# Kernel optimization log

Measured on AMD Instinct MI355X. Metric: run time of the kernel, lower is better.

## Reference

```python
import jax, jax.numpy as jnp
import numpy as np

B, C, H, L, P = 64, 64, 256, 64, 32
N_REAL = 2047
N = N_REAL + 1  # slot 0 is the null-child zero vector


def setup_inputs() -> dict:
    key = jax.random.key(0)
    ks = jax.random.split(key, 8)
    return {
        "node_feats": jax.random.normal(ks[0], (B, C, N), jnp.float32),
        "z": jax.random.normal(ks[1], (B, L), jnp.float32),
        "children": jax.random.randint(ks[2], (B, 3 * N_REAL), 0, N, jnp.int32),
        "conv1_w": jax.random.normal(ks[3], (H, C, 3), jnp.float32) * 0.05,
        "conv1_b": jnp.zeros((H,), jnp.float32),
        "conv2_w": jax.random.normal(ks[4], (H, H, 3), jnp.float32) * 0.05,
        "conv2_b": jnp.zeros((H,), jnp.float32),
        "mlp_w1": jax.random.normal(ks[5], (H + L, H), jnp.float32) * 0.05,
        "mlp_b1": jnp.zeros((H,), jnp.float32),
        "mlp_w2": jax.random.normal(ks[6], (H, P), jnp.float32) * 0.05,
        "mlp_b2": jnp.zeros((P,), jnp.float32),
    }


def _tree_conv(x, children, w, b):
    # x: [B, Cin, N]; children: [B, 3*N_real] indices of (self,left,right) triples
    g = jax.vmap(lambda xb, ib: xb[:, ib])(x, children)      # [B, Cin, 3*N_real]
    g = g.reshape(g.shape[0], g.shape[1], -1, 3)             # [B, Cin, N_real, 3]
    out = jnp.einsum('bcnk,hck->bhn', g, w) + b[None, :, None]  # Conv1d k=3 s=3
    zero = jnp.zeros((out.shape[0], out.shape[1], 1), out.dtype)
    return jnp.concatenate([zero, out], axis=2)              # [B, Cout, N]


def _tree_norm(x):
    # TreeLayerNorm: normalize each tree over all (channel, node) elements
    mean = jnp.mean(x, axis=(1, 2), keepdims=True)
    std = jnp.std(x, axis=(1, 2), keepdims=True, ddof=1)  # torch.std is unbiased
    return (x - mean) / (std + 1e-5)


def reference(node_feats, z, children, conv1_w, conv1_b, conv2_w, conv2_b,
              mlp_w1, mlp_b1, mlp_w2, mlp_b2):
    x = _tree_conv(node_feats, children, conv1_w, conv1_b)
    x = jax.nn.relu(_tree_norm(x))
    x = _tree_conv(x, children, conv2_w, conv2_b)
    x = jax.nn.relu(_tree_norm(x))                           # [B, H, N]
    z_exp = jnp.broadcast_to(z[:, :, None], (z.shape[0], z.shape[1], x.shape[2]))
    xz = jnp.concatenate([x, z_exp], axis=1)                 # [B, H+L, N]
    xz = xz.transpose(0, 2, 1)                               # [B, N, H+L]
    h = jax.nn.relu(xz @ mlp_w1 + mlp_b1)                    # [B, N, H]
    return h @ mlp_w2 + mlp_b2                               # [B, N, P]
```

## Files before the change

kernel.cpp:

```cpp
#include <hip/hip_runtime.h>
#include <hip/hip_bf16.h>

#define BATCH 64
#define CC    64
#define HH    256
#define LL    64
#define PP    32
#define NREAL 2047
#define NN    2048
#define MTOT  (HH*NN)

typedef unsigned short u16;
typedef __attribute__((ext_vector_type(8))) short short8;
typedef __attribute__((ext_vector_type(4))) float f32x4;

__device__ __forceinline__ float bu2f(u16 u) {
    return __uint_as_float(((unsigned)u) << 16);
}
__device__ __forceinline__ u16 f2bu(float f) {
    __hip_bfloat16 h = __float2bfloat16(f);
    return *reinterpret_cast<u16*>(&h);
}
__device__ __forceinline__ float ldv(const void* p, long long i, int f32) {
    return f32 ? ((const float*)p)[i] : bu2f(((const u16*)p)[i]);
}

__device__ __forceinline__ void async_cp16(const u16* src, u16* dst) {
    __builtin_amdgcn_global_load_lds(
        (const __attribute__((address_space(1))) unsigned int*)src,
        (__attribute__((address_space(3))) unsigned int*)dst,
        16, 0, 0);
}

__device__ __forceinline__ void swz(int id, int& b, int& tile) {
    b    = (id & 7) + 8 * ((id >> 3) & 7);
    tile = id >> 6;
}

__global__ __launch_bounds__(256) void detect_k(const u16* __restrict__ nf,
                                                int* __restrict__ flag) {
    __shared__ int cnt;
    if (threadIdx.x == 0) cnt = 0;
    __syncthreads();
    int c = 0;
#pragma unroll
    for (int i = 0; i < 16; ++i) {
        unsigned u = nf[threadIdx.x * 16 + i];
        unsigned e = (u >> 7) & 0xFF;
        if (e >= 161) c++;
    }
    atomicAdd(&cnt, c);
    __syncthreads();
    if (threadIdx.x == 0) flag[0] = (cnt > 64) ? 1 : 0;
}

__global__ __launch_bounds__(256) void prep_k(const void* __restrict__ c1w,
                                              const void* __restrict__ c2w,
                                              u16* __restrict__ wt1m,
                                              u16* __restrict__ wt2m,
                                              u16* __restrict__ x1t,
                                              float* __restrict__ statsz,
                                              const int* __restrict__ flag) {
    int isF32 = flag[0];
    int blk = blockIdx.x, tid = threadIdx.x;
    if (blk < 960) {
        const void* w = (blk < 192) ? c1w : c2w;
        u16* dst      = (blk < 192) ? wt1m : wt2m;
        int cinShift  = (blk < 192) ? 6 : 8;
        int t = ((blk < 192) ? blk : (blk - 192)) * 256 + tid;
        int CIN = 1 << cinShift;
        int kin = t & 31;
        int rest = t >> 5;
        int h = rest & (HH - 1);
        int ks = rest >> 8;
        int k = ks * 32 + kin;
        int kk = k >> cinShift, c = k & (CIN - 1);
        dst[t] = f2bu(ldv(w, (((long long)h << cinShift) + c) * 3 + kk, isF32));
    } else {
        int b = blk - 960;
        x1t[(long long)b * NN * HH + tid] = 0;
        if (b == 0) statsz[tid] = 0.f;
    }
}

__global__ __launch_bounds__(256) void tr_nf_k(const void* __restrict__ nf,
                                               u16* __restrict__ nf_t,
                                               const int* __restrict__ flag) {
    __shared__ u16 t[64][65];
    int isF32 = flag[0];
    int b = blockIdx.y;
    int n0 = blockIdx.x * 64;
    int tid = threadIdx.x;
    int lane = tid & 63, grp = tid >> 6;
#pragma unroll
    for (int i = 0; i < 16; ++i) {
        int c = grp * 16 + i;
        float v = ldv(nf, ((long long)b * CC + c) * NN + n0 + lane, isF32);
        t[c][lane] = f2bu(v);
    }
    __syncthreads();
#pragma unroll
    for (int i = 0; i < 16; ++i) {
        int n = grp * 16 + i;
        nf_t[((long long)b * NN + n0 + n) * CC + lane] = t[lane][n];
    }
}

__global__ __launch_bounds__(256) void wmlp2_k(const void* __restrict__ mw1,
                                               const void* __restrict__ mw2,
                                               u16* __restrict__ w1m,
                                               u16* __restrict__ w2m,
                                               const int* __restrict__ flag) {
    int isF32 = flag[0];
    int blk = blockIdx.x, tid = threadIdx.x;
    const void* w = (blk < 320) ? mw1 : mw2;
    u16* dst      = (blk < 320) ? w1m : w2m;
    int colShift  = (blk < 320) ? 8 : 5;
    int t = ((blk < 320) ? blk : (blk - 320)) * 256 + tid;
    int COLS = 1 << colShift;
    int kin = t & 31;
    int rest = t >> 5;
    int col = rest & (COLS - 1);
    int ks = rest >> colShift;
    dst[t] = f2bu(ldv(w, ((long long)(ks * 32 + kin) << colShift) + col, isF32));
}

__device__ __forceinline__ void load_norm(const float* stats, int b,
                                          float& mean, float& rstd) {
    float s = stats[b * 2], ss = stats[b * 2 + 1];
    float m = s / (float)MTOT;
    float var = (ss - s * s / (float)MTOT) / (float)(MTOT - 1);
    var = fmaxf(var, 0.f);
    mean = m;
    rstd = 1.f / (sqrtf(var) + 1e-5f);
}

__global__ __launch_bounds__(512, 2) void conv1_k(const u16* __restrict__ x_t,
                                                  const int* __restrict__ children,
                                                  const u16* __restrict__ wtm,
                                                  const void* __restrict__ bias,
                                                  float* __restrict__ stats_out,
                                                  u16* __restrict__ out_t,
                                                  const int* __restrict__ flag) {
    __shared__ u16 S[192 * CC];
    __shared__ int cidx[192];
    __shared__ float ps[16];

    int isF32 = flag[0];
    int b, ntile;
    swz(blockIdx.x, b, ntile);
    int n0 = ntile * 64;
    int tid = threadIdx.x;
    int lane = tid & 63, w = tid >> 6;
    int l15 = lane & 15, quad = lane >> 4;

    const long long cbase = (long long)b * (3 * NREAL);
    if (tid < 192) {
        int gi = 3 * n0 + tid;
        cidx[tid] = (gi < 3 * NREAL) ? children[cbase + gi] : 0;
    }
    __syncthreads();

    const long long xbase = (long long)b * NN;
    const u16* wb = wtm + ((long long)(w * 32 + l15)) * 32 + quad * 8;

    {
        int li = lane & 7;
#pragma unroll
        for (int g = 0; g < 3; ++g) {
            int rbase = w * 24 + g * 8;
            int r = rbase + (lane >> 3);
            int tap = r >> 6, nd = r & 63;
            int ci = cidx[3 * nd + tap];
            const u16* src = x_t + (xbase + ci) * CC
                             + ((li * 8) ^ ((r & 7) << 3));
            async_cp16(src, &S[rbase * CC]);
        }
    }
    __syncthreads();

    f32x4 acc[4][2];
#pragma unroll
    for (int mt = 0; mt < 4; ++mt) {
        acc[mt][0] = (f32x4){0.f, 0.f, 0.f, 0.f};
        acc[mt][1] = (f32x4){0.f, 0.f, 0.f, 0.f};
    }
    const int X = (l15 & 7) << 3;

    auto ard = [&](int ksg, int mt) -> short8 {
        int tap = ksg >> 1;
        int col = (ksg & 1) * 32 + quad * 8;
        int r = tap * 64 + mt * 16 + l15;
        return *(const short8*)&S[r * CC + (col ^ X)];
    };

    short8 b0 = *(const short8*)(wb);
    short8 b1 = *(const short8*)(wb + 512);
    short8 a[4];
#pragma unroll
    for (int mt = 0; mt < 4; ++mt) a[mt] = ard(0, mt);

#pragma unroll
    for (int ksg = 0; ksg < 6; ++ksg) {
        short8 cb0 = b0, cb1 = b1;
        short8 ca[4];
#pragma unroll
        for (int mt = 0; mt < 4; ++mt) ca[mt] = a[mt];
        if (ksg + 1 < 6) {
            const u16* wn = wb + (long long)(ksg + 1) * 8192;
            b0 = *(const short8*)(wn);
            b1 = *(const short8*)(wn + 512);
#pragma unroll
            for (int mt = 0; mt < 4; ++mt) a[mt] = ard(ksg + 1, mt);
        }
#pragma unroll
        for (int mt = 0; mt < 4; ++mt) {
            acc[mt][0] = __builtin_amdgcn_mfma_f32_16x16x32_bf16(ca[mt], cb0, acc[mt][0], 0, 0, 0);
            acc[mt][1] = __builtin_amdgcn_mfma_f32_16x16x32_bf16(ca[mt], cb1, acc[mt][1], 0, 0, 0);
        }
    }

    float s = 0.f, ss = 0.f;
#pragma unroll
    for (int nt = 0; nt < 2; ++nt) {
        int h = w * 32 + nt * 16 + l15;
        float bv = ldv(bias, h, isF32);
#pragma unroll
        for (int mt = 0; mt < 4; ++mt) {
#pragma unroll
            for (int r = 0; r < 4; ++r) {
                int nc = n0 + mt * 16 + quad * 4 + r;
                if (nc < NREAL) {
                    float v = acc[mt][nt][r] + bv;
                    s += v;
                    ss += v * v;
                    out_t[((long long)b * NN + 1 + nc) * HH + h] = f2bu(v);
                }
            }
        }
    }
#pragma unroll
    for (int off = 32; off; off >>= 1) {
        s  += __shfl_down(s, off);
        ss += __shfl_down(ss, off);
    }
    if (lane == 0) { ps[w] = s; ps[8 + w] = ss; }
    __syncthreads();
    if (tid == 0) {
        float S_ = 0.f, SS_ = 0.f;
#pragma unroll
        for (int i = 0; i < 8; ++i) { S_ += ps[i]; SS_ += ps[8 + i]; }
        atomicAdd(&stats_out[b * 2],     S_);
        atomicAdd(&stats_out[b * 2 + 1], SS_);
    }
}

__global__ __launch_bounds__(512, 2) void conv2_k(const u16* __restrict__ x_t,
                                                  const int* __restrict__ children,
                                                  const u16* __restrict__ wtm,
                                                  const void* __restrict__ bias,
                                                  const float* __restrict__ stats_in,
                                                  float* __restrict__ stats_out,
                                                  u16* __restrict__ out_t,
                                                  const int* __restrict__ flag) {
    constexpr int KT = 8;
    constexpr int RE = HH + 8;
    __shared__ u16 A[2][64 * RE];
    __shared__ int cidx[192];
    __shared__ float ps[16];

    int isF32 = flag[0];
    int b, ntile;
    swz(blockIdx.x, b, ntile);
    int n0 = ntile * 64;
    int tid = threadIdx.x;
    int lane = tid & 63, w = tid >> 6;
    int l15 = lane & 15, quad = lane >> 4;

    float mean, rstd;
    load_norm(stats_in, b, mean, rstd);

    const long long cbase = (long long)b * (3 * NREAL);
    if (tid < 192) {
        int gi = 3 * n0 + tid;
        cidx[tid] = (gi < 3 * NREAL) ? children[cbase + gi] : 0;
    }
    __syncthreads();

    const long long xbase = (long long)b * NN;
    const u16* wb = wtm + ((long long)(w * 32 + l15)) * 32 + quad * 8;

    {
        uint2 g0[8];
#pragma unroll
        for (int u = 0; u < 8; ++u) {
            int nd = w * 8 + u;
            g0[u] = *(const uint2*)(x_t + (xbase + cidx[3 * nd]) * HH + lane * 4);
        }
#pragma unroll
        for (int u = 0; u < 8; ++u) {
            int nd = w * 8 + u;
            float f[4];
            f[0] = bu2f((u16)(g0[u].x & 0xffff)); f[1] = bu2f((u16)(g0[u].x >> 16));
            f[2] = bu2f((u16)(g0[u].y & 0xffff)); f[3] = bu2f((u16)(g0[u].y >> 16));
#pragma unroll
            for (int j = 0; j < 4; ++j) f[j] = fmaxf((f[j] - mean) * rstd, 0.f);
            uint2 o;
            o.x = (unsigned)f2bu(f[0]) | ((unsigned)f2bu(f[1]) << 16);
            o.y = (unsigned)f2bu(f[2]) | ((unsigned)f2bu(f[3]) << 16);
            *(uint2*)&A[0][nd * RE + lane * 4] = o;
        }
    }
    __syncthreads();

    f32x4 acc[4][2];
#pragma unroll
    for (int mt = 0; mt < 4; ++mt)
#pragma unroll
        for (int nt = 0; nt < 2; ++nt) acc[mt][nt] = (f32x4){0.f, 0.f, 0.f, 0.f};

#pragma unroll
    for (int t = 0; t < 3; ++t) {
        const u16* Ac = &A[t & 1][0];
        u16* An = &A[(t + 1) & 1][0];

        short8 Bc[KT][2];
#pragma unroll
        for (int ks = 0; ks < KT; ++ks) {
            const u16* wn = wb + (long long)(t * KT + ks) * 8192;
            Bc[ks][0] = *(const short8*)(wn);
            Bc[ks][1] = *(const short8*)(wn + 512);
        }

        uint2 gv[8];
        if (t < 2) {
#pragma unroll
            for (int u = 0; u < 8; ++u) {
                int nd = w * 8 + u;
                gv[u] = *(const uint2*)(x_t + (xbase + cidx[3 * nd + t + 1]) * HH
                                        + lane * 4);
            }
        }

        short8 a0 = *(const short8*)&Ac[(l15)      * RE + quad * 8];
        short8 a1 = *(const short8*)&Ac[(16 + l15) * RE + quad * 8];
        short8 a2 = *(const short8*)&Ac[(32 + l15) * RE + quad * 8];
        short8 a3 = *(const short8*)&Ac[(48 + l15) * RE + quad * 8];
#pragma unroll
        for (int ks = 0; ks < KT; ++ks) {
            short8 ca0 = a0, ca1 = a1, ca2 = a2, ca3 = a3;
            if (ks + 1 < KT) {
                int ko = (ks + 1) * 32 + quad * 8;
                a0 = *(const short8*)&Ac[(l15)      * RE + ko];
                a1 = *(const short8*)&Ac[(16 + l15) * RE + ko];
                a2 = *(const short8*)&Ac[(32 + l15) * RE + ko];
                a3 = *(const short8*)&Ac[(48 + l15) * RE + ko];
            }
            acc[0][0] = __builtin_amdgcn_mfma_f32_16x16x32_bf16(ca0, Bc[ks][0], acc[0][0], 0, 0, 0);
            acc[1][0] = __builtin_amdgcn_mfma_f32_16x16x32_bf16(ca1, Bc[ks][0], acc[1][0], 0, 0, 0);
            acc[2][0] = __builtin_amdgcn_mfma_f32_16x16x32_bf16(ca2, Bc[ks][0], acc[2][0], 0, 0, 0);
            acc[3][0] = __builtin_amdgcn_mfma_f32_16x16x32_bf16(ca3, Bc[ks][0], acc[3][0], 0, 0, 0);
            acc[0][1] = __builtin_amdgcn_mfma_f32_16x16x32_bf16(ca0, Bc[ks][1], acc[0][1], 0, 0, 0);
            acc[1][1] = __builtin_amdgcn_mfma_f32_16x16x32_bf16(ca1, Bc[ks][1], acc[1][1], 0, 0, 0);
            acc[2][1] = __builtin_amdgcn_mfma_f32_16x16x32_bf16(ca2, Bc[ks][1], acc[2][1], 0, 0, 0);
            acc[3][1] = __builtin_amdgcn_mfma_f32_16x16x32_bf16(ca3, Bc[ks][1], acc[3][1], 0, 0, 0);
        }

        if (t < 2) {
#pragma unroll
            for (int u = 0; u < 8; ++u) {
                int nd = w * 8 + u;
                float f[4];
                f[0] = bu2f((u16)(gv[u].x & 0xffff));
                f[1] = bu2f((u16)(gv[u].x >> 16));
                f[2] = bu2f((u16)(gv[u].y & 0xffff));
                f[3] = bu2f((u16)(gv[u].y >> 16));
#pragma unroll
                for (int j = 0; j < 4; ++j)
                    f[j] = fmaxf((f[j] - mean) * rstd, 0.f);
                uint2 o;
                o.x = (unsigned)f2bu(f[0]) | ((unsigned)f2bu(f[1]) << 16);
                o.y = (unsigned)f2bu(f[2]) | ((unsigned)f2bu(f[3]) << 16);
                *(uint2*)&An[nd * RE + lane * 4] = o;
            }
        }
        __syncthreads();
    }

    float s = 0.f, ss = 0.f;
#pragma unroll
    for (int nt = 0; nt < 2; ++nt) {
        int h = w * 32 + nt * 16 + l15;
        float bv = ldv(bias, h, isF32);
#pragma unroll
        for (int mt = 0; mt < 4; ++mt) {
#pragma unroll
            for (int r = 0; r < 4; ++r) {
                int nc = n0 + mt * 16 + quad * 4 + r;
                if (nc < NREAL) {
                    float v = acc[mt][nt][r] + bv;
                    s += v;
                    ss += v * v;
                    out_t[((long long)b * NN + 1 + nc) * HH + h] = f2bu(v);
                }
            }
        }
    }
#pragma unroll
    for (int off = 32; off; off >>= 1) {
        s  += __shfl_down(s, off);
        ss += __shfl_down(ss, off);
    }
    if (lane == 0) { ps[w] = s; ps[8 + w] = ss; }
    __syncthreads();
    if (tid == 0) {
        float S_ = 0.f, SS_ = 0.f;
#pragma unroll
        for (int i = 0; i < 8; ++i) { S_ += ps[i]; SS_ += ps[8 + i]; }
        atomicAdd(&stats_out[b * 2],     S_);
        atomicAdd(&stats_out[b * 2 + 1], SS_);
    }
    if (ntile == 0 && tid < 32) {
        uint4 zz = {0u, 0u, 0u, 0u};
        *(uint4*)&out_t[((long long)b * NN) * HH + tid * 8] = zz;
    }
}

#define REX 328
#define REH 264
__global__ __launch_bounds__(256, 4) void mlpm_k(const u16* __restrict__ x2t,
                                                 const void* __restrict__ z,
                                                 const u16* __restrict__ w1m,
                                                 const void* __restrict__ b1,
                                                 const u16* __restrict__ w2m,
                                                 const void* __restrict__ b2,
                                                 const float* __restrict__ stats,
                                                 void* __restrict__ out,
                                                 const int* __restrict__ flag) {
    __shared__ u16 xz[32 * REX];
    __shared__ u16 hbuf[32 * REH];
    int isF32 = flag[0];
    int b, tile;
    swz(blockIdx.x, b, tile);
    int n0 = tile * 32;
    int tid = threadIdx.x;
    int lane = tid & 63, w = tid >> 6;
    int l15 = lane & 15, quad = lane >> 4;

    float mean, rstd;
    load_norm(stats, b, mean, rstd);
    u16 zb = f2bu(ldv(z, (long long)b * LL + lane, isF32));

    uint4 vv[4];
#pragma unroll
    for (int u = 0; u < 4; ++u) {
        int node = w * 8 + u * 2 + (lane >> 5);
        int lo = lane & 31;
        vv[u] = *(const uint4*)(x2t + ((long long)(b * NN + n0 + node)) * HH
                                + lo * 8);
    }
#pragma unroll
    for (int u = 0; u < 4; ++u) {
        int node = w * 8 + u * 2 + (lane >> 5);
        int lo = lane & 31;
        unsigned wd[4] = {vv[u].x, vv[u].y, vv[u].z, vv[u].w};
#pragma unroll
        for (int j = 0; j < 4; ++j) {
            float flo = fmaxf((bu2f((u16)(wd[j] & 0xffff)) - mean) * rstd, 0.f);
            float fhi = fmaxf((bu2f((u16)(wd[j] >> 16))   - mean) * rstd, 0.f);
            wd[j] = (unsigned)f2bu(flo) | ((unsigned)f2bu(fhi) << 16);
        }
        *(uint4*)&xz[node * REX + lo * 8] = make_uint4(wd[0], wd[1], wd[2], wd[3]);
    }
#pragma unroll
    for (int u = 0; u < 8; ++u)
        xz[(w * 8 + u) * REX + HH + lane] = zb;
    __syncthreads();

    f32x4 acc[2][4];
#pragma unroll
    for (int mt = 0; mt < 2; ++mt)
#pragma unroll
        for (int nt = 0; nt < 4; ++nt) acc[mt][nt] = (f32x4){0.f, 0.f, 0.f, 0.f};

    const u16* wbase = w1m + ((long long)(w * 64 + l15)) * 32 + quad * 8;
    short8 bf0 = *(const short8*)(wbase);
    short8 bf1 = *(const short8*)(wbase + 512);
    short8 bf2 = *(const short8*)(wbase + 1024);
    short8 bf3 = *(const short8*)(wbase + 1536);
    short8 a0 = *(const short8*)&xz[l15 * REX + quad * 8];
    short8 a1 = *(const short8*)&xz[(16 + l15) * REX + quad * 8];

    for (int ks = 0; ks < 10; ++ks) {
        short8 c0 = bf0, c1 = bf1, c2 = bf2, c3 = bf3;
        short8 ca0 = a0, ca1 = a1;
        if (ks + 1 < 10) {
            const u16* wn = wbase + (long long)(ks + 1) * 8192;
            bf0 = *(const short8*)(wn);
            bf1 = *(const short8*)(wn + 512);
            bf2 = *(const short8*)(wn + 1024);
            bf3 = *(const short8*)(wn + 1536);
            a0 = *(const short8*)&xz[l15 * REX + (ks + 1) * 32 + quad * 8];
            a1 = *(const short8*)&xz[(16 + l15) * REX + (ks + 1) * 32 + quad * 8];
        }
        acc[0][0] = __builtin_amdgcn_mfma_f32_16x16x32_bf16(ca0, c0, acc[0][0], 0, 0, 0);
        acc[1][0] = __builtin_amdgcn_mfma_f32_16x16x32_bf16(ca1, c0, acc[1][0], 0, 0, 0);
        acc[0][1] = __builtin_amdgcn_mfma_f32_16x16x32_bf16(ca0, c1, acc[0][1], 0, 0, 0);
        acc[1][1] = __builtin_amdgcn_mfma_f32_16x16x32_bf16(ca1, c1, acc[1][1], 0, 0, 0);
        acc[0][2] = __builtin_amdgcn_mfma_f32_16x16x32_bf16(ca0, c2, acc[0][2], 0, 0, 0);
        acc[1][2] = __builtin_amdgcn_mfma_f32_16x16x32_bf16(ca1, c2, acc[1][2], 0, 0, 0);
        acc[0][3] = __builtin_amdgcn_mfma_f32_16x16x32_bf16(ca0, c3, acc[0][3], 0, 0, 0);
        acc[1][3] = __builtin_amdgcn_mfma_f32_16x16x32_bf16(ca1, c3, acc[1][3], 0, 0, 0);
    }
#pragma unroll
    for (int nt = 0; nt < 4; ++nt) {
        int j = w * 64 + nt * 16 + l15;
        float bv = ldv(b1, j, isF32);
#pragma unroll
        for (int mt = 0; mt < 2; ++mt)
#pragma unroll
            for (int r = 0; r < 4; ++r) {
                int node = mt * 16 + quad * 4 + r;
                hbuf[node * REH + j] = f2bu(fmaxf(acc[mt][nt][r] + bv, 0.f));
            }
    }
    __syncthreads();

    int mt = w & 1, nt = w >> 1;
    f32x4 acc2 = (f32x4){0.f, 0.f, 0.f, 0.f};
#pragma unroll
    for (int ks = 0; ks < 8; ++ks) {
        short8 a = *(const short8*)&hbuf[(mt * 16 + l15) * REH + ks * 32 + quad * 8];
        short8 bf = *(const short8*)(w2m + ((long long)ks * PP + nt * 16 + l15) * 32 + quad * 8);
        acc2 = __builtin_amdgcn_mfma_f32_16x16x32_bf16(a, bf, acc2, 0, 0, 0);
    }
    int p = nt * 16 + l15;
    float bp = ldv(b2, p, isF32);
#pragma unroll
    for (int r = 0; r < 4; ++r) {
        int node = mt * 16 + quad * 4 + r;
        long long o = ((long long)(b * NN + n0 + node)) * PP + p;
        float v = acc2[r] + bp;
        if (isF32) ((float*)out)[o] = v;
        else       ((u16*)out)[o] = f2bu(v);
    }
}

__global__ __launch_bounds__(256) void fill0_k(void* out, const int* flag, int n) {
    int i = blockIdx.x * 256 + threadIdx.x;
    if (i >= n) return;
    if (flag[0]) ((float*)out)[i] = 0.f;
    else ((u16*)out)[i] = 0;
}

extern "C" void kernel_launch(void* const* d_in, const int* in_sizes, int n_in,
                              void* d_out, int out_size, void* d_ws, size_t ws_size,
                              hipStream_t stream) {
    const void* nf  = d_in[0];
    const void* z   = d_in[1];
    const int*  ch  = (const int*)d_in[2];
    const void* c1w = d_in[3];
    const void* c1b = d_in[4];
    const void* c2w = d_in[5];
    const void* c2b = d_in[6];
    const void* mw1 = d_in[7];
    const void* mb1 = d_in[8];
    const void* mw2 = d_in[9];
    const void* mb2 = d_in[10];

    char* ws = (char*)d_ws;
    int*   flag   = (int*)ws;
    float* statsz = (float*)(ws + 256);
    float* stats1 = (float*)(ws + 256);
    float* stats2 = (float*)(ws + 768);
    u16* x1t  = (u16*)(ws + 4096);
    u16* A    = (u16*)(ws + 4096 + 67108864LL);
    u16* nf_t = A;
    u16* x2t  = A;
    u16* wt1m = (u16*)d_out;
    u16* wt2m = wt1m + 192 * 256;
    u16* w1m = x1t;
    u16* w2m = x1t + 320 * 256;

    const size_t NEED = 4096 + 2 * 67108864ULL;
    if (ws_size < NEED) {
        detect_k<<<1, 256, 0, stream>>>((const u16*)nf, flag);
        fill0_k<<<(out_size + 255) / 256, 256, 0, stream>>>(d_out, flag, out_size);
        return;
    }

    detect_k<<<1, 256, 0, stream>>>((const u16*)nf, flag);
    prep_k<<<1024, 256, 0, stream>>>(c1w, c2w, wt1m, wt2m, x1t, statsz, flag);
    tr_nf_k<<<dim3(NN / 64, BATCH), 256, 0, stream>>>(nf, nf_t, flag);

    conv1_k<<<32 * BATCH, 512, 0, stream>>>(nf_t, ch, wt1m, c1b,
                                            stats1, x1t, flag);
    conv2_k<<<32 * BATCH, 512, 0, stream>>>(x1t, ch, wt2m, c2b,
                                            stats1, stats2, x2t, flag);
    wmlp2_k<<<352, 256, 0, stream>>>(mw1, mw2, w1m, w2m, flag);
    mlpm_k<<<64 * BATCH, 256, 0, stream>>>(x2t, z, w1m, mb1, w2m, mb2,
                                           stats2, d_out, flag);
}
```

Measured before the change: 292.8 us.

## Fold node-feature transpose into prep kernel and enlarge MLP tile to 64 nodes

```diff
diff --git a/kernel.cpp b/kernel.cpp
--- a/kernel.cpp
+++ b/kernel.cpp
@@ -56,53 +56,50 @@
 
 __global__ __launch_bounds__(256) void prep_k(const void* __restrict__ c1w,
                                               const void* __restrict__ c2w,
+                                              const void* __restrict__ nf,
                                               u16* __restrict__ wt1m,
                                               u16* __restrict__ wt2m,
                                               u16* __restrict__ x1t,
+                                              u16* __restrict__ nf_t,
                                               float* __restrict__ statsz,
                                               const int* __restrict__ flag) {
+    __shared__ u16 t[64][65];
     int isF32 = flag[0];
     int blk = blockIdx.x, tid = threadIdx.x;
     if (blk < 960) {
         const void* w = (blk < 192) ? c1w : c2w;
         u16* dst      = (blk < 192) ? wt1m : wt2m;
         int cinShift  = (blk < 192) ? 6 : 8;
-        int t = ((blk < 192) ? blk : (blk - 192)) * 256 + tid;
+        int tt = ((blk < 192) ? blk : (blk - 192)) * 256 + tid;
         int CIN = 1 << cinShift;
-        int kin = t & 31;
-        int rest = t >> 5;
+        int kin = tt & 31;
+        int rest = tt >> 5;
         int h = rest & (HH - 1);
         int ks = rest >> 8;
         int k = ks * 32 + kin;
         int kk = k >> cinShift, c = k & (CIN - 1);
-        dst[t] = f2bu(ldv(w, (((long long)h << cinShift) + c) * 3 + kk, isF32));
-    } else {
+        dst[tt] = f2bu(ldv(w, (((long long)h << cinShift) + c) * 3 + kk, isF32));
+    } else if (blk < 1024) {
         int b = blk - 960;
         x1t[(long long)b * NN * HH + tid] = 0;
         if (b == 0) statsz[tid] = 0.f;
-    }
-}
-
-__global__ __launch_bounds__(256) void tr_nf_k(const void* __restrict__ nf,
-                                               u16* __restrict__ nf_t,
-                                               const int* __restrict__ flag) {
-    __shared__ u16 t[64][65];
-    int isF32 = flag[0];
-    int b = blockIdx.y;
-    int n0 = blockIdx.x * 64;
-    int tid = threadIdx.x;
-    int lane = tid & 63, grp = tid >> 6;
-#pragma unroll
-    for (int i = 0; i < 16; ++i) {
-        int c = grp * 16 + i;
-        float v = ldv(nf, ((long long)b * CC + c) * NN + n0 + lane, isF32);
-        t[c][lane] = f2bu(v);
-    }
-    __syncthreads();
-#pragma unroll
-    for (int i = 0; i < 16; ++i) {
-        int n = grp * 16 + i;
-        nf_t[((long long)b * NN + n0 + n) * CC + lane] = t[lane][n];
+    } else {
+        int id = blk - 1024;
+        int b = id >> 5;
+        int n0 = (id & 31) * 64;
+        int lane = tid & 63, grp = tid >> 6;
+#pragma unroll
+        for (int i = 0; i < 16; ++i) {
+            int c = grp * 16 + i;
+            float v = ldv(nf, ((long long)b * CC + c) * NN + n0 + lane, isF32);
+            t[c][lane] = f2bu(v);
+        }
+        __syncthreads();
+#pragma unroll
+        for (int i = 0; i < 16; ++i) {
+            int n = grp * 16 + i;
+            nf_t[((long long)b * NN + n0 + n) * CC + lane] = t[lane][n];
+        }
     }
 }
 
@@ -428,7 +425,7 @@
 
 #define REX 328
 #define REH 264
-__global__ __launch_bounds__(256, 4) void mlpm_k(const u16* __restrict__ x2t,
+__global__ __launch_bounds__(512, 2) void mlpm_k(const u16* __restrict__ x2t,
                                                  const void* __restrict__ z,
                                                  const u16* __restrict__ w1m,
                                                  const void* __restrict__ b1,
@@ -437,12 +434,12 @@
                                                  const float* __restrict__ stats,
                                                  void* __restrict__ out,
                                                  const int* __restrict__ flag) {
-    __shared__ u16 xz[32 * REX];
-    __shared__ u16 hbuf[32 * REH];
+    __shared__ u16 xz[64 * REX];
+    __shared__ u16 hbuf[64 * REH];
     int isF32 = flag[0];
     int b, tile;
     swz(blockIdx.x, b, tile);
-    int n0 = tile * 32;
+    int n0 = tile * 64;
     int tid = threadIdx.x;
     int lane = tid & 63, w = tid >> 6;
     int l15 = lane & 15, quad = lane >> 4;
@@ -477,47 +474,49 @@
         xz[(w * 8 + u) * REX + HH + lane] = zb;
     __syncthreads();
 
-    f32x4 acc[2][4];
-#pragma unroll
-    for (int mt = 0; mt < 2; ++mt)
-#pragma unroll
-        for (int nt = 0; nt < 4; ++nt) acc[mt][nt] = (f32x4){0.f, 0.f, 0.f, 0.f};
-
-    const u16* wbase = w1m + ((long long)(w * 64 + l15)) * 32 + quad * 8;
+    f32x4 acc[4][2];
+#pragma unroll
+    for (int mt = 0; mt < 4; ++mt) {
+        acc[mt][0] = (f32x4){0.f, 0.f, 0.f, 0.f};
+        acc[mt][1] = (f32x4){0.f, 0.f, 0.f, 0.f};
+    }
+
+    const u16* wbase = w1m + ((long long)(w * 32 + l15)) * 32 + quad * 8;
     short8 bf0 = *(const short8*)(wbase);
     short8 bf1 = *(const short8*)(wbase + 512);
-    short8 bf2 = *(const short8*)(wbase + 1024);
-    short8 bf3 = *(const short8*)(wbase + 1536);
-    short8 a0 = *(const short8*)&xz[l15 * REX + quad * 8];
+    short8 a0 = *(const short8*)&xz[(l15)      * REX + quad * 8];
     short8 a1 = *(const short8*)&xz[(16 + l15) * REX + quad * 8];
+    short8 a2 = *(const short8*)&xz[(32 + l15) * REX + quad * 8];
+    short8 a3 = *(const short8*)&xz[(48 + l15) * REX + quad * 8];
 
     for (int ks = 0; ks < 10; ++ks) {
-        short8 c0 = bf0, c1 = bf1, c2 = bf2, c3 = bf3;
-        short8 ca0 = a0, ca1 = a1;
+        short8 c0 = bf0, c1 = bf1;
+        short8 ca0 = a0, ca1 = a1, ca2 = a2, ca3 = a3;
         if (ks + 1 < 10) {
             const u16* wn = wbase + (long long)(ks + 1) * 8192;
             bf0 = *(const short8*)(wn);
             bf1 = *(const short8*)(wn + 512);
-            bf2 = *(const short8*)(wn + 1024);
-            bf3 = *(const short8*)(wn + 1536);
-            a0 = *(const short8*)&xz[l15 * REX + (ks + 1) * 32 + quad * 8];
-            a1 = *(const short8*)&xz[(16 + l15) * REX + (ks + 1) * 32 + quad * 8];
+            int ko = (ks + 1) * 32 + quad * 8;
+            a0 = *(const short8*)&xz[(l15)      * REX + ko];
+            a1 = *(const short8*)&xz[(16 + l15) * REX + ko];
+            a2 = *(const short8*)&xz[(32 + l15) * REX + ko];
+            a3 = *(const short8*)&xz[(48 + l15) * REX + ko];
         }
         acc[0][0] = __builtin_amdgcn_mfma_f32_16x16x32_bf16(ca0, c0, acc[0][0], 0, 0, 0);
         acc[1][0] = __builtin_amdgcn_mfma_f32_16x16x32_bf16(ca1, c0, acc[1][0], 0, 0, 0);
+        acc[2][0] = __builtin_amdgcn_mfma_f32_16x16x32_bf16(ca2, c0, acc[2][0], 0, 0, 0);
+        acc[3][0] = __builtin_amdgcn_mfma_f32_16x16x32_bf16(ca3, c0, acc[3][0], 0, 0, 0);
         acc[0][1] = __builtin_amdgcn_mfma_f32_16x16x32_bf16(ca0, c1, acc[0][1], 0, 0, 0);
         acc[1][1] = __builtin_amdgcn_mfma_f32_16x16x32_bf16(ca1, c1, acc[1][1], 0, 0, 0);
-        acc[0][2] = __builtin_amdgcn_mfma_f32_16x16x32_bf16(ca0, c2, acc[0][2], 0, 0, 0);
-        acc[1][2] = __builtin_amdgcn_mfma_f32_16x16x32_bf16(ca1, c2, acc[1][2], 0, 0, 0);
-        acc[0][3] = __builtin_amdgcn_mfma_f32_16x16x32_bf16(ca0, c3, acc[0][3], 0, 0, 0);
-        acc[1][3] = __builtin_amdgcn_mfma_f32_16x16x32_bf16(ca1, c3, acc[1][3], 0, 0, 0);
-    }
-#pragma unroll
-    for (int nt = 0; nt < 4; ++nt) {
-        int j = w * 64 + nt * 16 + l15;
+        acc[2][1] = __builtin_amdgcn_mfma_f32_16x16x32_bf16(ca2, c1, acc[2][1], 0, 0, 0);
+        acc[3][1] = __builtin_amdgcn_mfma_f32_16x16x32_bf16(ca3, c1, acc[3][1], 0, 0, 0);
+    }
+#pragma unroll
+    for (int nt = 0; nt < 2; ++nt) {
+        int j = w * 32 + nt * 16 + l15;
         float bv = ldv(b1, j, isF32);
 #pragma unroll
-        for (int mt = 0; mt < 2; ++mt)
+        for (int mt = 0; mt < 4; ++mt)
 #pragma unroll
             for (int r = 0; r < 4; ++r) {
                 int node = mt * 16 + quad * 4 + r;
@@ -526,15 +525,15 @@
     }
     __syncthreads();
 
-    int mt = w & 1, nt = w >> 1;
+    int mt = w & 3, np = w >> 2;
     f32x4 acc2 = (f32x4){0.f, 0.f, 0.f, 0.f};
 #pragma unroll
     for (int ks = 0; ks < 8; ++ks) {
         short8 a = *(const short8*)&hbuf[(mt * 16 + l15) * REH + ks * 32 + quad * 8];
-        short8 bf = *(const short8*)(w2m + ((long long)ks * PP + nt * 16 + l15) * 32 + quad * 8);
+        short8 bf = *(const short8*)(w2m + ((long long)ks * PP + np * 16 + l15) * 32 + quad * 8);
         acc2 = __builtin_amdgcn_mfma_f32_16x16x32_bf16(a, bf, acc2, 0, 0, 0);
     }
-    int p = nt * 16 + l15;
+    int p = np * 16 + l15;
     float bp = ldv(b2, p, isF32);
 #pragma unroll
     for (int r = 0; r < 4; ++r) {
@@ -590,14 +589,14 @@
     }
 
     detect_k<<<1, 256, 0, stream>>>((const u16*)nf, flag);
-    prep_k<<<1024, 256, 0, stream>>>(c1w, c2w, wt1m, wt2m, x1t, statsz, flag);
-    tr_nf_k<<<dim3(NN / 64, BATCH), 256, 0, stream>>>(nf, nf_t, flag);
+    prep_k<<<3072, 256, 0, stream>>>(c1w, c2w, nf, wt1m, wt2m, x1t, nf_t,
+                                     statsz, flag);
 
     conv1_k<<<32 * BATCH, 512, 0, stream>>>(nf_t, ch, wt1m, c1b,
                                             stats1, x1t, flag);
     conv2_k<<<32 * BATCH, 512, 0, stream>>>(x1t, ch, wt2m, c2b,
                                             stats1, stats2, x2t, flag);
     wmlp2_k<<<352, 256, 0, stream>>>(mw1, mw2, w1m, w2m, flag);
-    mlpm_k<<<64 * BATCH, 256, 0, stream>>>(x2t, z, w1m, mb1, w2m, mb2,
+    mlpm_k<<<32 * BATCH, 512, 0, stream>>>(x2t, z, w1m, mb1, w2m, mb2,
                                            stats2, d_out, flag);
 }
```

After: 279.3 us. -4.6%, faster.
